# Optimization experiments

Hardware: AMD Instinct MI355X
Metric: run time of the kernel (lower is better)

The kernel has to match this reference:

```python
import math
import jax, jax.numpy as jnp
import numpy as np

B, S, D, H = 4, 2048, 1024, 16
HD = D // H  # head_dim = 64


def setup_inputs() -> dict:
    key = jax.random.key(0)
    ks = jax.random.split(key, 10)
    scale = 1.0 / math.sqrt(D)
    inp = {
        "q": jax.random.normal(ks[0], (B, S, D), dtype=jnp.float32),
        "q_mask": jax.random.bernoulli(ks[1], 0.9, (B, S)),
        "Wq": jax.random.normal(ks[2], (D, D), dtype=jnp.float32) * scale,
        "bq": jax.random.normal(ks[3], (D,), dtype=jnp.float32) * 0.01,
        "Wk": jax.random.normal(ks[4], (D, D), dtype=jnp.float32) * scale,
        "bk": jax.random.normal(ks[5], (D,), dtype=jnp.float32) * 0.01,
        "Wv": jax.random.normal(ks[6], (D, D), dtype=jnp.float32) * scale,
        "bv": jax.random.normal(ks[7], (D,), dtype=jnp.float32) * 0.01,
        "Wo": jax.random.normal(ks[8], (D, D), dtype=jnp.float32) * scale,
        "bo": jax.random.normal(ks[9], (D,), dtype=jnp.float32) * 0.01,
    }
    return inp


def reference(q, q_mask, Wq, bq, Wk, bk, Wv, bv, Wo, bo):
    # Self-attention: k = v = q, kv_mask = q_mask (per forward() defaults).
    # Linear projections (nn.Linear: x @ W^T + b), then split heads -> (b, h, s, hd)
    def proj(x, W, b):
        y = jnp.einsum("bsd,ed->bse", x, W) + b
        return y.reshape(B, S, H, HD).transpose(0, 2, 1, 3)

    qh = proj(q, Wq, bq)
    kh = proj(q, Wk, bk)
    vh = proj(q, Wv, bv)

    # Scaled dot-product scores: (b, h, s_q, s_k), scaled by sqrt(head_dim)
    scores = jnp.einsum("bhqd,bhkd->bhqk", qh, kh) / math.sqrt(HD)

    # merge_masks: q_mask & kv_mask (kv_mask == q_mask), broadcast over heads
    merged = q_mask[:, :, None] & q_mask[:, None, :]          # (b, s_q, s_k)
    scores = jnp.where(merged[:, None, :, :], scores, -jnp.inf)

    # softmax over keys; fully-masked (padded query) rows -> nan -> 0
    attn = jax.nn.softmax(scores, axis=-1)
    attn = jnp.nan_to_num(attn, nan=0.0)
    # dropout prob = 0 (eval) -> no-op

    out = jnp.einsum("bhqk,bhkd->bhqd", attn, vh)             # (b, h, s, hd)
    out = out.transpose(0, 2, 1, 3).reshape(B, S, D)
    return jnp.einsum("bsd,ed->bse", out, Wo) + bo
```

## Files before the change

kernel.cpp:

```cpp
#include <hip/hip_runtime.h>
#include <hip/hip_bf16.h>
#include <stdint.h>

typedef __bf16 v8y __attribute__((ext_vector_type(8)));
typedef _Float16 v8h __attribute__((ext_vector_type(8)));
typedef float  v4f __attribute__((ext_vector_type(4)));
typedef float  v16f __attribute__((ext_vector_type(16)));
typedef unsigned u32x2 __attribute__((ext_vector_type(2)));
typedef __hip_bfloat16 bf;

#define AS1 __attribute__((address_space(1)))
#define AS3 __attribute__((address_space(3)))

__device__ __forceinline__ void gload16(const bf* g, bf* l) {
  __builtin_amdgcn_global_load_lds((const AS1 uint32_t*)g, (AS3 uint32_t*)l, 16, 0, 0);
}

static constexpr int Bb = 4, Sdim = 2048, Ddim = 1024, Hn = 16, HD = 64;
static constexpr int Kd = 1024, Nd = 1024;
static constexpr int WSZ = Ddim * Ddim;
static constexpr float NEG = -1e30f;

__device__ __forceinline__ void stc(bf* p, float v)    { *p = __float2bfloat16(v); }
__device__ __forceinline__ void stc(float* p, float v) { *p = v; }

__device__ __forceinline__ uint32_t pkbf(float lo, float hi_) {
  union { bf h[2]; uint32_t u; } t;
  t.h[0] = __float2bfloat16(lo);
  t.h[1] = __float2bfloat16(hi_);
  return t.u;
}

__device__ __forceinline__ void plswap(uint32_t& a, uint32_t& b) {
  u32x2 r = __builtin_amdgcn_permlane32_swap(a, b, false, false);
  a = r.x; b = r.y;
}

__device__ __forceinline__ float xhalf(float x, int hi) {
  uint32_t a = __builtin_bit_cast(uint32_t, x), b = a;
  plswap(a, b);
  return __builtin_bit_cast(float, hi ? a : b);
}

__global__ __launch_bounds__(256)
void cvt_f16(const float* __restrict__ src, uint16_t* __restrict__ dst, int n) {
  const int i = (blockIdx.x * 256 + threadIdx.x) * 8;
  if (i >= n) return;
  const float4 a = *reinterpret_cast<const float4*>(src + i);
  const float4 b = *reinterpret_cast<const float4*>(src + i + 4);
  const float x[8] = {a.x, a.y, a.z, a.w, b.x, b.y, b.z, b.w};
  union { uint16_t h[8]; uint4 u; } U;
#pragma unroll
  for (int j = 0; j < 8; ++j) U.h[j] = __builtin_bit_cast(uint16_t, (_Float16)x[j]);
  *reinterpret_cast<uint4*>(dst + i) = U.u;
}

__global__ __launch_bounds__(256)
void cvt_w(const float* __restrict__ Wq, const float* __restrict__ Wk,
           const float* __restrict__ Wv, const float* __restrict__ Wo,
           uint16_t* __restrict__ wb) {
  const int i = (blockIdx.x * 256 + threadIdx.x) * 8;
  const int z = blockIdx.y;
  const float* src = z == 0 ? Wq : (z == 1 ? Wk : (z == 2 ? Wv : Wo));
  uint16_t* dst = wb + (size_t)WSZ * z;
  const float4 a = *reinterpret_cast<const float4*>(src + i);
  const float4 b = *reinterpret_cast<const float4*>(src + i + 4);
  const float x[8] = {a.x, a.y, a.z, a.w, b.x, b.y, b.z, b.w};
  union { uint16_t h[8]; uint4 u; } U;
  if (z < 3) {
#pragma unroll
    for (int j = 0; j < 8; ++j) U.h[j] = __builtin_bit_cast(uint16_t, (_Float16)x[j]);
  } else {
#pragma unroll
    for (int j = 0; j < 8; ++j) U.h[j] = __builtin_bit_cast(uint16_t, __float2bfloat16(x[j]));
  }
  *reinterpret_cast<uint4*>(dst + i) = U.u;
}

__global__ __launch_bounds__(256)
void maskpack(const int* __restrict__ mask, uint64_t* __restrict__ mp) {
  const int gid = blockIdx.x * 256 + threadIdx.x;
  const uint64_t bal = __ballot(mask[gid] != 0);
  if ((threadIdx.x & 63) == 0) mp[gid >> 6] = bal;
}

template<bool F16, bool HEADLAYOUT, typename TC>
__global__ __launch_bounds__(256)
void gemm_bt(const bf* __restrict__ A,
             const bf* __restrict__ W0, const bf* __restrict__ W1, const bf* __restrict__ W2,
             const float* __restrict__ b0, const float* __restrict__ b1, const float* __restrict__ b2,
             TC* __restrict__ C0, TC* __restrict__ C1, TC* __restrict__ C2)
{
  const int z = blockIdx.z;
  const bf* Wh = z == 0 ? W0 : (z == 1 ? W1 : W2);
  const float* bias = z == 0 ? b0 : (z == 1 ? b1 : b2);
  TC* C = z == 0 ? C0 : (z == 1 ? C1 : C2);

  constexpr int PL = 128 * 32;
  __shared__ __align__(16) bf As[PL];
  __shared__ __align__(16) bf Bs[PL];

  const int tid = threadIdx.x;
  const int w = tid >> 6, l = tid & 63;
  const int m0 = blockIdx.x * 128, n0 = blockIdx.y * 128;
  const int wm = (w & 1) * 64, wn = (w >> 1) * 64;
  const int lr = l & 15, quad = l >> 4;
  const int srow = l >> 2, sk = (l & 3) * 8;

  v4f acc[4][4] = {};

  for (int kt = 0; kt < Kd; kt += 32) {
    __syncthreads();
#pragma unroll
    for (int c = 0; c < 2; ++c) {
      const int rb = (c * 4 + w) * 16;
      const int64_t goff = (int64_t)(rb + srow) * Kd + kt + sk;
      gload16(A + (int64_t)m0 * Kd + goff, As + rb * 32);
      gload16(Wh + (int64_t)n0 * Kd + goff, Bs + rb * 32);
    }
    __syncthreads();

    v8y afh[4], bfh[4];
#pragma unroll
    for (int i = 0; i < 4; ++i) {
      const int ro = (wm + i * 16 + lr) * 32 + quad * 8;
      const int co = (wn + i * 16 + lr) * 32 + quad * 8;
      afh[i] = *reinterpret_cast<const v8y*>(As + ro);
      bfh[i] = *reinterpret_cast<const v8y*>(Bs + co);
    }
#pragma unroll
    for (int i = 0; i < 4; ++i)
#pragma unroll
      for (int j = 0; j < 4; ++j) {
        if constexpr (F16) {
          acc[i][j] = __builtin_amdgcn_mfma_f32_16x16x32_f16(
              __builtin_bit_cast(v8h, afh[i]), __builtin_bit_cast(v8h, bfh[j]),
              acc[i][j], 0, 0, 0);
        } else {
          acc[i][j] = __builtin_amdgcn_mfma_f32_16x16x32_bf16(afh[i], bfh[j], acc[i][j], 0, 0, 0);
        }
      }
  }

#pragma unroll
  for (int j = 0; j < 4; ++j) {
    const int gn = n0 + wn + j * 16 + lr;
    const float bv = bias[gn];
#pragma unroll
    for (int i = 0; i < 4; ++i) {
#pragma unroll
      for (int r = 0; r < 4; ++r) {
        const int gm = m0 + wm + i * 16 + quad * 4 + r;
        float v = acc[i][j][r] + bv;
        if (HEADLAYOUT) {
          const int bidx = gm >> 11, s = gm & (Sdim - 1);
          const int h = gn >> 6, hd = gn & (HD - 1);
          if (z == 0) v *= 0.125f;
          const int64_t idx = (z == 2)
            ? ((int64_t)(bidx * Hn + h) * HD + hd) * Sdim + s
            : (((int64_t)(bidx * Hn + h) * Sdim + s) << 6) + hd;
          stc(&C[idx], v);
        } else {
          stc(&C[(int64_t)gm * Nd + gn], v);
        }
      }
    }
  }
}

__global__ __launch_bounds__(256)
void attn_kernel(const bf* __restrict__ qh, const bf* __restrict__ kh,
                 const bf* __restrict__ vt, const int* __restrict__ mask,
                 const uint64_t* __restrict__ mp, bf* __restrict__ outp)
{
  __shared__ __align__(16) bf sm[2][8192];

  const int tid = threadIdx.x;
  const int w = tid >> 6, l = tid & 63;
  const int lq = l & 31, hi = l >> 5;
  const int bh = blockIdx.x, b = bh >> 4;
  const int q0 = blockIdx.y * 128 + w * 32;
  const int64_t base = (int64_t)bh * (Sdim * HD);

  v8y qf[4];
#pragma unroll
  for (int s = 0; s < 4; ++s)
    qf[s] = *reinterpret_cast<const v8y*>(qh + base + (int64_t)(q0 + lq) * 64 + s * 16 + hi * 8);

  const bool qmask = mask[b * Sdim + q0 + lq] != 0;

  float m_i = NEG, l_i = 0.f;
  v16f oacc[2] = {};

  const int srcperm = ((l & 7) ^ (l >> 3)) * 8;
  const int srow8 = l >> 3;

#define STAGE(bufi, ktn)                                                          \
  {                                                                               \
    bf* KB_ = sm[bufi];                                                           \
    bf* VB_ = sm[bufi] + 4096;                                                    \
    _Pragma("unroll")                                                             \
    for (int i_ = 0; i_ < 2; ++i_) {                                              \
      const int c_ = w * 2 + i_;                                                  \
      const int row_ = c_ * 8 + srow8;                                            \
      gload16(kh + base + (int64_t)((ktn) + row_) * 64 + srcperm, KB_ + c_ * 512);\
      gload16(vt + base + (int64_t)row_ * Sdim + (ktn) + srcperm, VB_ + c_ * 512);\
    }                                                                             \
  }

  STAGE(0, 0);
  asm volatile("s_waitcnt vmcnt(0)" ::: "memory");
  __syncthreads();

  for (int kt = 0; kt < Sdim; kt += 64) {
    const int buf = (kt >> 6) & 1;
    if (kt + 64 < Sdim) STAGE(buf ^ 1, kt + 64);

    const bf* KB = sm[buf];
    const bf* VB = sm[buf] + 4096;

    v16f sacc[2] = {};
    __builtin_amdgcn_s_setprio(1);
#pragma unroll
    for (int n = 0; n < 2; ++n) {
      const int row = n * 32 + lq;
      const int swz = (row & 7);
#pragma unroll
      for (int s = 0; s < 4; ++s) {
        const int colE = ((2 * s + hi) ^ swz) * 8;
        v8y kf = *reinterpret_cast<const v8y*>(KB + row * 64 + colE);
        sacc[n] = __builtin_amdgcn_mfma_f32_32x32x16_bf16(kf, qf[s], sacc[n], 0, 0, 0);
      }
    }
    __builtin_amdgcn_s_setprio(0);

    const uint64_t km64 = mp[b * 32 + (kt >> 6)];
    const uint32_t km0 = (uint32_t)km64 >> (4 * hi);
    const uint32_t km1 = (uint32_t)(km64 >> 32) >> (4 * hi);
#pragma unroll
    for (int r = 0; r < 16; ++r) {
      const uint32_t bit = 1u << ((r & 3) + 8 * (r >> 2));
      sacc[0][r] = (km0 & bit) ? sacc[0][r] : NEG;
      sacc[1][r] = (km1 & bit) ? sacc[1][r] : NEG;
    }

    float mxc[4] = {NEG, NEG, NEG, NEG};
#pragma unroll
    for (int n = 0; n < 2; ++n)
#pragma unroll
      for (int r = 0; r < 16; r += 4) {
#pragma unroll
        for (int c = 0; c < 4; ++c) mxc[c] = fmaxf(mxc[c], sacc[n][r + c]);
      }
    float mx = fmaxf(fmaxf(mxc[0], mxc[1]), fmaxf(mxc[2], mxc[3]));
    mx = fmaxf(mx, xhalf(mx, hi));
    const float mn = fmaxf(m_i, mx);
    const float alpha = __expf(m_i - mn);
    m_i = mn;

#pragma unroll
    for (int n = 0; n < 2; ++n)
#pragma unroll
      for (int r = 0; r < 16; ++r) sacc[n][r] = __expf(sacc[n][r] - mn);

    float smc[4] = {0.f, 0.f, 0.f, 0.f};
#pragma unroll
    for (int n = 0; n < 2; ++n)
#pragma unroll
      for (int r = 0; r < 16; r += 4) {
#pragma unroll
        for (int c = 0; c < 4; ++c) smc[c] += sacc[n][r + c];
      }
    float sum = (smc[0] + smc[1]) + (smc[2] + smc[3]);
    sum += xhalf(sum, hi);
    l_i = l_i * alpha + sum;
#pragma unroll
    for (int d2 = 0; d2 < 2; ++d2)
#pragma unroll
      for (int r = 0; r < 16; ++r) oacc[d2][r] *= alpha;

    uint32_t pq[8][2];
#pragma unroll
    for (int n = 0; n < 2; ++n)
#pragma unroll
      for (int g = 0; g < 4; ++g) {
        pq[n * 4 + g][0] = pkbf(sacc[n][g * 4 + 0], sacc[n][g * 4 + 1]);
        pq[n * 4 + g][1] = pkbf(sacc[n][g * 4 + 2], sacc[n][g * 4 + 3]);
      }

#pragma unroll
    for (int ks = 0; ks < 4; ++ks) {
      plswap(pq[2 * ks][0], pq[2 * ks + 1][0]);
      plswap(pq[2 * ks][1], pq[2 * ks + 1][1]);
    }

#pragma unroll
    for (int ks = 0; ks < 4; ++ks) {
      union { uint32_t u[4]; v8y v; } pf;
      pf.u[0] = pq[2 * ks][0];
      pf.u[1] = pq[2 * ks][1];
      pf.u[2] = pq[2 * ks + 1][0];
      pf.u[3] = pq[2 * ks + 1][1];
      __builtin_amdgcn_s_setprio(1);
#pragma unroll
      for (int d2 = 0; d2 < 2; ++d2) {
        const int row = d2 * 32 + lq;
        const int colE = ((2 * ks + hi) ^ (row & 7)) * 8;
        v8y vf = *reinterpret_cast<const v8y*>(VB + row * 64 + colE);
        oacc[d2] = __builtin_amdgcn_mfma_f32_32x32x16_bf16(vf, pf.v, oacc[d2], 0, 0, 0);
      }
      __builtin_amdgcn_s_setprio(0);
    }

    asm volatile("s_waitcnt vmcnt(0)" ::: "memory");
    __syncthreads();
  }
#undef STAGE

  const float inv = qmask ? 1.f / l_i : 0.f;
  bf* orow = outp + ((int64_t)b * Sdim + q0 + lq) * Ddim + (bh & 15) * 64;
#pragma unroll
  for (int d2 = 0; d2 < 2; ++d2)
#pragma unroll
    for (int g = 0; g < 4; ++g) {
      union { bf h[4]; uint2 u; } pk;
#pragma unroll
      for (int c = 0; c < 4; ++c) pk.h[c] = __float2bfloat16(oacc[d2][g * 4 + c] * inv);
      *reinterpret_cast<uint2*>(orow + d2 * 32 + 8 * g + 4 * hi) = pk.u;
    }
}

extern "C" void kernel_launch(void* const* d_in, const int* in_sizes, int n_in,
                              void* d_out, int out_size, void* d_ws, size_t ws_size,
                              hipStream_t stream) {
  (void)in_sizes; (void)n_in; (void)out_size; (void)ws_size;
  const float* q    = (const float*)d_in[0];
  const int*   mask = (const int*)d_in[1];
  const float* Wq = (const float*)d_in[2];
  const float* bq = (const float*)d_in[3];
  const float* Wk = (const float*)d_in[4];
  const float* bk = (const float*)d_in[5];
  const float* Wv = (const float*)d_in[6];
  const float* bv = (const float*)d_in[7];
  const float* Wo = (const float*)d_in[8];
  const float* bo = (const float*)d_in[9];
  float* out = (float*)d_out;
  bf* ws  = (bf*)d_ws;

  constexpr int SZ = Bb * Sdim * Ddim;

  bf* qc  = ws;
  bf* qhp = ws + (size_t)SZ;
  bf* khp = ws + 2 * (size_t)SZ;
  bf* vtp = ws + 3 * (size_t)SZ;
  bf* wb  = ws + 4 * (size_t)SZ;
  bf* wq = wb;
  bf* wk = wb + WSZ;
  bf* wv = wb + 2 * (size_t)WSZ;
  bf* wo = wb + 3 * (size_t)WSZ;
  uint64_t* mpk = (uint64_t*)(wb + 4 * (size_t)WSZ);
  bf* ao = qc;

  cvt_f16<<<dim3(SZ / 2048), dim3(256), 0, stream>>>(q, (uint16_t*)qc, SZ);
  cvt_w<<<dim3(WSZ / 2048, 4), dim3(256), 0, stream>>>(Wq, Wk, Wv, Wo, (uint16_t*)wb);
  maskpack<<<dim3(32), dim3(256), 0, stream>>>(mask, mpk);

  gemm_bt<true, true, bf><<<dim3(64, 8, 3), dim3(256), 0, stream>>>(
      qc, wq, wk, wv, bq, bk, bv, qhp, khp, vtp);

  attn_kernel<<<dim3(Bb * Hn, Sdim / 128), dim3(256), 0, stream>>>(qhp, khp, vtp, mask, mpk, ao);

  gemm_bt<false, false, float><<<dim3(64, 8, 1), dim3(256), 0, stream>>>(
      ao, wo, wo, wo, bo, bo, bo, out, out, out);
}
```

Before: 349.9 us.

## Use exp2 softmax with lazy rescaling and packed f32x2 ops in attention

The change folds log2(e) into the Q projection scale so the softmax can use exp2f directly instead of __expf. It also skips the running-max update and the output accumulator rescale whenever no lane's new max exceeds the old one by more than a threshold. The subtract and sum steps are rewritten on f32x2 vectors so the compiler can emit packed FP32 instructions. The aim is to cut VALU work in the softmax between the MFMA phases, with a bounded growth of unnormalised values as the trade-off.

```diff
diff --git a/kernel.cpp b/kernel.cpp
--- a/kernel.cpp
+++ b/kernel.cpp
@@ -6,6 +6,7 @@
 typedef _Float16 v8h __attribute__((ext_vector_type(8)));
 typedef float  v4f __attribute__((ext_vector_type(4)));
 typedef float  v16f __attribute__((ext_vector_type(16)));
+typedef float  f32x2 __attribute__((ext_vector_type(2)));
 typedef unsigned u32x2 __attribute__((ext_vector_type(2)));
 typedef __hip_bfloat16 bf;
 
@@ -20,6 +21,7 @@
 static constexpr int Kd = 1024, Nd = 1024;
 static constexpr int WSZ = Ddim * Ddim;
 static constexpr float NEG = -1e30f;
+static constexpr float QSCALE = 0.18033688011112042f;
 
 __device__ __forceinline__ void stc(bf* p, float v)    { *p = __float2bfloat16(v); }
 __device__ __forceinline__ void stc(float* p, float v) { *p = v; }
@@ -155,7 +157,7 @@
         if (HEADLAYOUT) {
           const int bidx = gm >> 11, s = gm & (Sdim - 1);
           const int h = gn >> 6, hd = gn & (HD - 1);
-          if (z == 0) v *= 0.125f;
+          if (z == 0) v *= QSCALE;
           const int64_t idx = (z == 2)
             ? ((int64_t)(bidx * Hn + h) * HD + hd) * Sdim + s
             : (((int64_t)(bidx * Hn + h) * Sdim + s) << 6) + hd;
@@ -190,7 +192,9 @@
   const bool qmask = mask[b * Sdim + q0 + lq] != 0;
 
   float m_i = NEG, l_i = 0.f;
-  v16f oacc[2] = {};
+  union V16 { v16f v; f32x2 p[8]; };
+  V16 oacc[2];
+  oacc[0].v = {}; oacc[1].v = {};
 
   const int srcperm = ((l & 7) ^ (l >> 3)) * 8;
   const int srow8 = l >> 3;
@@ -219,7 +223,8 @@
     const bf* KB = sm[buf];
     const bf* VB = sm[buf] + 4096;
 
-    v16f sacc[2] = {};
+    V16 sacc[2];
+    sacc[0].v = {}; sacc[1].v = {};
     __builtin_amdgcn_s_setprio(1);
 #pragma unroll
     for (int n = 0; n < 2; ++n) {
@@ -229,7 +234,7 @@
       for (int s = 0; s < 4; ++s) {
         const int colE = ((2 * s + hi) ^ swz) * 8;
         v8y kf = *reinterpret_cast<const v8y*>(KB + row * 64 + colE);
-        sacc[n] = __builtin_amdgcn_mfma_f32_32x32x16_bf16(kf, qf[s], sacc[n], 0, 0, 0);
+        sacc[n].v = __builtin_amdgcn_mfma_f32_32x32x16_bf16(kf, qf[s], sacc[n].v, 0, 0, 0);
       }
     }
     __builtin_amdgcn_s_setprio(0);
@@ -240,8 +245,8 @@
 #pragma unroll
     for (int r = 0; r < 16; ++r) {
       const uint32_t bit = 1u << ((r & 3) + 8 * (r >> 2));
-      sacc[0][r] = (km0 & bit) ? sacc[0][r] : NEG;
-      sacc[1][r] = (km1 & bit) ? sacc[1][r] : NEG;
+      sacc[0].v[r] = (km0 & bit) ? sacc[0].v[r] : NEG;
+      sacc[1].v[r] = (km1 & bit) ? sacc[1].v[r] : NEG;
     }
 
     float mxc[4] = {NEG, NEG, NEG, NEG};
@@ -250,42 +255,47 @@
 #pragma unroll
       for (int r = 0; r < 16; r += 4) {
 #pragma unroll
-        for (int c = 0; c < 4; ++c) mxc[c] = fmaxf(mxc[c], sacc[n][r + c]);
+        for (int c = 0; c < 4; ++c) mxc[c] = fmaxf(mxc[c], sacc[n].v[r + c]);
       }
     float mx = fmaxf(fmaxf(mxc[0], mxc[1]), fmaxf(mxc[2], mxc[3]));
     mx = fmaxf(mx, xhalf(mx, hi));
-    const float mn = fmaxf(m_i, mx);
-    const float alpha = __expf(m_i - mn);
-    m_i = mn;
-
-#pragma unroll
-    for (int n = 0; n < 2; ++n)
-#pragma unroll
-      for (int r = 0; r < 16; ++r) sacc[n][r] = __expf(sacc[n][r] - mn);
-
-    float smc[4] = {0.f, 0.f, 0.f, 0.f};
-#pragma unroll
-    for (int n = 0; n < 2; ++n)
-#pragma unroll
-      for (int r = 0; r < 16; r += 4) {
-#pragma unroll
-        for (int c = 0; c < 4; ++c) smc[c] += sacc[n][r + c];
-      }
-    float sum = (smc[0] + smc[1]) + (smc[2] + smc[3]);
+
+    if (!__all(mx - m_i <= 11.0f)) {
+      const float mn = fmaxf(m_i, mx);
+      const float alpha = exp2f(m_i - mn);
+      m_i = mn;
+      l_i *= alpha;
+      const f32x2 a2 = {alpha, alpha};
+#pragma unroll
+      for (int i = 0; i < 8; ++i) { oacc[0].p[i] *= a2; oacc[1].p[i] *= a2; }
+    }
+
+    const f32x2 m2 = {m_i, m_i};
+#pragma unroll
+    for (int n = 0; n < 2; ++n)
+#pragma unroll
+      for (int i = 0; i < 8; ++i) sacc[n].p[i] -= m2;
+#pragma unroll
+    for (int n = 0; n < 2; ++n)
+#pragma unroll
+      for (int r = 0; r < 16; ++r) sacc[n].v[r] = exp2f(sacc[n].v[r]);
+
+    f32x2 sc0 = {0.f, 0.f}, sc1 = {0.f, 0.f};
+#pragma unroll
+    for (int n = 0; n < 2; ++n)
+#pragma unroll
+      for (int i = 0; i < 8; i += 2) { sc0 += sacc[n].p[i]; sc1 += sacc[n].p[i + 1]; }
+    float sum = (sc0.x + sc0.y) + (sc1.x + sc1.y);
     sum += xhalf(sum, hi);
-    l_i = l_i * alpha + sum;
-#pragma unroll
-    for (int d2 = 0; d2 < 2; ++d2)
-#pragma unroll
-      for (int r = 0; r < 16; ++r) oacc[d2][r] *= alpha;
+    l_i += sum;
 
     uint32_t pq[8][2];
 #pragma unroll
     for (int n = 0; n < 2; ++n)
 #pragma unroll
       for (int g = 0; g < 4; ++g) {
-        pq[n * 4 + g][0] = pkbf(sacc[n][g * 4 + 0], sacc[n][g * 4 + 1]);
-        pq[n * 4 + g][1] = pkbf(sacc[n][g * 4 + 2], sacc[n][g * 4 + 3]);
+        pq[n * 4 + g][0] = pkbf(sacc[n].v[g * 4 + 0], sacc[n].v[g * 4 + 1]);
+        pq[n * 4 + g][1] = pkbf(sacc[n].v[g * 4 + 2], sacc[n].v[g * 4 + 3]);
       }
 
 #pragma unroll
@@ -307,7 +317,7 @@
         const int row = d2 * 32 + lq;
         const int colE = ((2 * ks + hi) ^ (row & 7)) * 8;
         v8y vf = *reinterpret_cast<const v8y*>(VB + row * 64 + colE);
-        oacc[d2] = __builtin_amdgcn_mfma_f32_32x32x16_bf16(vf, pf.v, oacc[d2], 0, 0, 0);
+        oacc[d2].v = __builtin_amdgcn_mfma_f32_32x32x16_bf16(vf, pf.v, oacc[d2].v, 0, 0, 0);
       }
       __builtin_amdgcn_s_setprio(0);
     }
@@ -325,7 +335,7 @@
     for (int g = 0; g < 4; ++g) {
       union { bf h[4]; uint2 u; } pk;
 #pragma unroll
-      for (int c = 0; c < 4; ++c) pk.h[c] = __float2bfloat16(oacc[d2][g * 4 + c] * inv);
+      for (int c = 0; c < 4; ++c) pk.h[c] = __float2bfloat16(oacc[d2].v[g * 4 + c] * inv);
       *reinterpret_cast<uint2*>(orow + d2 * 32 + 8 * g + 4 * hi) = pk.u;
     }
 }
```

Result: slower. 362.8 us (+3.7%).

## Replace projection GEMMs with 256x256 double-buffered swizzled-LDS kernel

Applied to the files above, without the earlier changes.

Replaces the 128x128, 256-thread GEMM with a 256x256-tile, 512-thread kernel that uses BK=64, a double-buffered 128KB LDS, and an XOR swizzle on the LDS layout. The next K tile is prefetched with global_load_lds while MFMAs run, and s_setprio raises wave priority during the MFMA blocks. The aim is more data reuse per tile, no global-load stalls, and fewer LDS bank conflicts. In exchange, far fewer blocks are launched (384 and 128), which may leave CUs idle, and each thread holds more registers.

```diff
diff --git a/kernel.cpp b/kernel.cpp
--- a/kernel.cpp
+++ b/kernel.cpp
@@ -40,6 +40,15 @@
   uint32_t a = __builtin_bit_cast(uint32_t, x), b = a;
   plswap(a, b);
   return __builtin_bit_cast(float, hi ? a : b);
+}
+
+template<bool F16>
+__device__ __forceinline__ v4f mf(v8y a, v8y b, v4f c) {
+  if constexpr (F16)
+    return __builtin_amdgcn_mfma_f32_16x16x32_f16(
+        __builtin_bit_cast(v8h, a), __builtin_bit_cast(v8h, b), c, 0, 0, 0);
+  else
+    return __builtin_amdgcn_mfma_f32_16x16x32_bf16(a, b, c, 0, 0, 0);
 }
 
 __global__ __launch_bounds__(256)
@@ -85,8 +94,8 @@
 }
 
 template<bool F16, bool HEADLAYOUT, typename TC>
-__global__ __launch_bounds__(256)
-void gemm_bt(const bf* __restrict__ A,
+__global__ __launch_bounds__(512, 2)
+void gemm256(const bf* __restrict__ A,
              const bf* __restrict__ W0, const bf* __restrict__ W1, const bf* __restrict__ W2,
              const float* __restrict__ b0, const float* __restrict__ b1, const float* __restrict__ b2,
              TC* __restrict__ C0, TC* __restrict__ C1, TC* __restrict__ C2)
@@ -96,62 +105,114 @@
   const float* bias = z == 0 ? b0 : (z == 1 ? b1 : b2);
   TC* C = z == 0 ? C0 : (z == 1 ? C1 : C2);
 
-  constexpr int PL = 128 * 32;
-  __shared__ __align__(16) bf As[PL];
-  __shared__ __align__(16) bf Bs[PL];
+  __shared__ __align__(16) bf sm[65536];
 
   const int tid = threadIdx.x;
   const int w = tid >> 6, l = tid & 63;
-  const int m0 = blockIdx.x * 128, n0 = blockIdx.y * 128;
-  const int wm = (w & 1) * 64, wn = (w >> 1) * 64;
+  const int wr = w >> 2, wc = w & 3;
   const int lr = l & 15, quad = l >> 4;
-  const int srow = l >> 2, sk = (l & 3) * 8;
-
-  v4f acc[4][4] = {};
-
-  for (int kt = 0; kt < Kd; kt += 32) {
+  const int m0 = blockIdx.x * 256, n0 = blockIdx.y * 256;
+
+  const int sr = w * 8 + (l >> 3);
+  const int sperm = ((l & 7) ^ (l >> 3)) * 8;
+  const int swz = l & 7;
+
+  v4f acc[8][4] = {};
+
+#define ST64(G, R0, KT, LB) \
+  gload16((G) + (int64_t)((R0) + sr) * Kd + (KT) + (sperm), sm + (LB) + w * 512)
+
+#pragma unroll
+  for (int c = 0; c < 4; ++c) {
+    ST64(A,  m0 + c * 64, 0, c * 4096);
+    ST64(Wh, n0 + c * 64, 0, 16384 + c * 4096);
+  }
+  __syncthreads();
+
+  for (int t = 0; t < 16; ++t) {
+    const int d = t & 1;
+    const bf* Ab = sm + d * 32768;
+    const bf* Bb = Ab + 16384;
+    const int lb = (d ^ 1) * 32768;
+    const int ktn = (t + 1) * 64;
+    const bool pf = t < 15;
+
+    v8y af[4], bfr[4];
+
+#pragma unroll
+    for (int n = 0; n < 4; ++n)
+      bfr[n] = *reinterpret_cast<const v8y*>(Bb + (wc * 64 + n * 16 + lr) * 64 + ((quad) ^ swz) * 8);
+#pragma unroll
+    for (int m = 0; m < 4; ++m)
+      af[m] = *reinterpret_cast<const v8y*>(Ab + (wr * 128 + m * 16 + lr) * 64 + ((quad) ^ swz) * 8);
+    if (pf) {
+#pragma unroll
+      for (int c = 0; c < 4; ++c) ST64(A, m0 + c * 64, ktn, lb + c * 4096);
+    }
+    __builtin_amdgcn_s_barrier();
+    __builtin_amdgcn_s_setprio(1);
+#pragma unroll
+    for (int m = 0; m < 4; ++m)
+#pragma unroll
+      for (int n = 0; n < 4; ++n) acc[m][n] = mf<F16>(af[m], bfr[n], acc[m][n]);
+    __builtin_amdgcn_s_setprio(0);
+    __builtin_amdgcn_s_barrier();
+
+#pragma unroll
+    for (int m = 0; m < 4; ++m)
+      af[m] = *reinterpret_cast<const v8y*>(Ab + (wr * 128 + (m + 4) * 16 + lr) * 64 + ((quad) ^ swz) * 8);
+    if (pf) {
+#pragma unroll
+      for (int c = 0; c < 4; ++c) ST64(Wh, n0 + c * 64, ktn, lb + 16384 + c * 4096);
+    }
+    __builtin_amdgcn_s_barrier();
+    __builtin_amdgcn_s_setprio(1);
+#pragma unroll
+    for (int m = 0; m < 4; ++m)
+#pragma unroll
+      for (int n = 0; n < 4; ++n) acc[m + 4][n] = mf<F16>(af[m], bfr[n], acc[m + 4][n]);
+    __builtin_amdgcn_s_setprio(0);
+    __builtin_amdgcn_s_barrier();
+
+#pragma unroll
+    for (int n = 0; n < 4; ++n)
+      bfr[n] = *reinterpret_cast<const v8y*>(Bb + (wc * 64 + n * 16 + lr) * 64 + ((4 + quad) ^ swz) * 8);
+#pragma unroll
+    for (int m = 0; m < 4; ++m)
+      af[m] = *reinterpret_cast<const v8y*>(Ab + (wr * 128 + m * 16 + lr) * 64 + ((4 + quad) ^ swz) * 8);
+    __builtin_amdgcn_s_barrier();
+    __builtin_amdgcn_s_setprio(1);
+#pragma unroll
+    for (int m = 0; m < 4; ++m)
+#pragma unroll
+      for (int n = 0; n < 4; ++n) acc[m][n] = mf<F16>(af[m], bfr[n], acc[m][n]);
+    __builtin_amdgcn_s_setprio(0);
+    __builtin_amdgcn_s_barrier();
+
+#pragma unroll
+    for (int m = 0; m < 4; ++m)
+      af[m] = *reinterpret_cast<const v8y*>(Ab + (wr * 128 + (m + 4) * 16 + lr) * 64 + ((4 + quad) ^ swz) * 8);
+    __builtin_amdgcn_s_barrier();
+    __builtin_amdgcn_s_setprio(1);
+#pragma unroll
+    for (int m = 0; m < 4; ++m)
+#pragma unroll
+      for (int n = 0; n < 4; ++n) acc[m + 4][n] = mf<F16>(af[m], bfr[n], acc[m + 4][n]);
+    __builtin_amdgcn_s_setprio(0);
     __syncthreads();
-#pragma unroll
-    for (int c = 0; c < 2; ++c) {
-      const int rb = (c * 4 + w) * 16;
-      const int64_t goff = (int64_t)(rb + srow) * Kd + kt + sk;
-      gload16(A + (int64_t)m0 * Kd + goff, As + rb * 32);
-      gload16(Wh + (int64_t)n0 * Kd + goff, Bs + rb * 32);
-    }
-    __syncthreads();
-
-    v8y afh[4], bfh[4];
-#pragma unroll
-    for (int i = 0; i < 4; ++i) {
-      const int ro = (wm + i * 16 + lr) * 32 + quad * 8;
-      const int co = (wn + i * 16 + lr) * 32 + quad * 8;
-      afh[i] = *reinterpret_cast<const v8y*>(As + ro);
-      bfh[i] = *reinterpret_cast<const v8y*>(Bs + co);
-    }
-#pragma unroll
-    for (int i = 0; i < 4; ++i)
-#pragma unroll
-      for (int j = 0; j < 4; ++j) {
-        if constexpr (F16) {
-          acc[i][j] = __builtin_amdgcn_mfma_f32_16x16x32_f16(
-              __builtin_bit_cast(v8h, afh[i]), __builtin_bit_cast(v8h, bfh[j]),
-              acc[i][j], 0, 0, 0);
-        } else {
-          acc[i][j] = __builtin_amdgcn_mfma_f32_16x16x32_bf16(afh[i], bfh[j], acc[i][j], 0, 0, 0);
-        }
-      }
-  }
-
-#pragma unroll
-  for (int j = 0; j < 4; ++j) {
-    const int gn = n0 + wn + j * 16 + lr;
+  }
+#undef ST64
+
+#pragma unroll
+  for (int n = 0; n < 4; ++n) {
+    const int gn = n0 + wc * 64 + n * 16 + lr;
     const float bv = bias[gn];
 #pragma unroll
-    for (int i = 0; i < 4; ++i) {
+    for (int m = 0; m < 8; ++m) {
 #pragma unroll
       for (int r = 0; r < 4; ++r) {
-        const int gm = m0 + wm + i * 16 + quad * 4 + r;
-        float v = acc[i][j][r] + bv;
+        const int gm = m0 + wr * 128 + m * 16 + quad * 4 + r;
+        float v = acc[m][n][r] + bv;
         if (HEADLAYOUT) {
           const int bidx = gm >> 11, s = gm & (Sdim - 1);
           const int h = gn >> 6, hd = gn & (HD - 1);
@@ -365,11 +426,11 @@
   cvt_w<<<dim3(WSZ / 2048, 4), dim3(256), 0, stream>>>(Wq, Wk, Wv, Wo, (uint16_t*)wb);
   maskpack<<<dim3(32), dim3(256), 0, stream>>>(mask, mpk);
 
-  gemm_bt<true, true, bf><<<dim3(64, 8, 3), dim3(256), 0, stream>>>(
+  gemm256<true, true, bf><<<dim3(32, 4, 3), dim3(512), 0, stream>>>(
       qc, wq, wk, wv, bq, bk, bv, qhp, khp, vtp);
 
   attn_kernel<<<dim3(Bb * Hn, Sdim / 128), dim3(256), 0, stream>>>(qhp, khp, vtp, mask, mpk, ao);
 
-  gemm_bt<false, false, float><<<dim3(64, 8, 1), dim3(256), 0, stream>>>(
+  gemm256<false, false, float><<<dim3(32, 4, 1), dim3(512), 0, stream>>>(
       ao, wo, wo, wo, bo, bo, bo, out, out, out);
 }
```

Result: slower. 371.6 us (+6.2%).
